# Kernel tuning notes

Hardware: AMD Instinct MI355X
Metric: run time of the kernel (lower is better)

The kernel has to match this reference:

```python
import jax, jax.numpy as jnp
import numpy as np

K = 3  # kernel size


def _qparams(t):
    # dynamic per-tensor affine quant params: scale=(max-min)/255, zero=-round(min/scale)
    mx = jnp.max(t)
    mn = jnp.min(t)
    s = (mx - mn) / 255.0
    z = -jnp.round(mn / s)
    return s, z


def _quant(t, s, z):
    return jnp.clip(jnp.round(t / s + z), 0.0, 255.0).astype(jnp.int32)


def setup_inputs() -> dict:
    key = jax.random.key(0)
    k1, k2, k3 = jax.random.split(key, 3)
    x = jax.random.normal(k1, (4, 32, 34, 34), dtype=jnp.float32)
    weight = jax.random.normal(k2, (64, 32, K, K), dtype=jnp.float32) * 0.1
    bias = jax.random.normal(k3, (64,), dtype=jnp.float32) * 0.1
    a = jnp.arange(256, dtype=jnp.float32)
    lut = a[:, None] * a[None, :]
    return {"x": x, "weight": weight, "lut": lut, "bias": bias}


def reference(x, weight, lut, bias):
    OC = weight.shape[0]
    # --- dynamic per-tensor quantization of activations and weights ---
    s_x, z_x = _qparams(x)
    s_w, z_w = _qparams(weight)
    qx = _quant(x, s_x, z_x)                       # [B, C, H, W] uint8 codes (int32)
    qw = _quant(weight, s_w, z_w).reshape(OC, -1)  # [OC, C*K*K]

    # --- im2col on the quantized activations (VALID, stride 1) ---
    patches = jax.lax.conv_general_dilated_patches(
        qx.astype(jnp.float32), (K, K), (1, 1), 'VALID')  # [B, C*K*K, OH, OW]
    B, CKK, OH, OW = patches.shape
    qxp = patches.astype(jnp.int32).transpose(0, 2, 3, 1).reshape(B, OH * OW, CKK)

    # --- LUT-based approximate multiply-accumulate ---
    # idx[b, p, oc, k] = qxp[b, p, k] * 256 + qw[oc, k]
    idx = qxp[:, :, None, :] * 256 + qw[None, None, :, :]          # [B, P, OC, CKK]
    acc = jnp.take(lut.reshape(-1), idx).sum(axis=-1)              # [B, P, OC]

    # --- affine dequantization of the integer accumulator ---
    sum_qw = qw.sum(axis=-1).astype(jnp.float32)                   # [OC]
    sum_qx = qxp.sum(axis=-1).astype(jnp.float32)                  # [B, P]
    out = s_x * s_w * (acc
                       - z_x * sum_qw[None, None, :]
                       - z_w * sum_qx[:, :, None]
                       + CKK * z_x * z_w)                          # [B, P, OC]
    out = out.reshape(B, OH, OW, OC).transpose(0, 3, 1, 2)         # [B, OC, OH, OW]
    return out + bias[None, :, None, None]
```

## Files before the change

kernel.cpp:

```cpp
#include <hip/hip_runtime.h>
#include <stdint.h>

#define B_    4
#define C_    32
#define HW_   34
#define OC_   64
#define CKK_  288

#define NX (B_*C_*HW_*HW_)
#define NW (OC_*C_*9)
#define NX4 (NX/4)
#define NW4 (NW/4)
#define NT4 (NX4+NW4)

__device__ __forceinline__ unsigned fmap(float f) {
  int i = __float_as_int(f);
  return (i < 0) ? ~(unsigned)i : ((unsigned)i | 0x80000000u);
}
__device__ __forceinline__ float funmap(unsigned u) {
  int i = (u & 0x80000000u) ? (int)(u ^ 0x80000000u) : ~(int)u;
  return __int_as_float(i);
}
__device__ __forceinline__ unsigned umax_(unsigned a, unsigned b){ return a>b?a:b; }
__device__ __forceinline__ unsigned umin_(unsigned a, unsigned b){ return a<b?a:b; }

__device__ __forceinline__ unsigned dot4(unsigned a, unsigned b, unsigned acc) {
#if __has_builtin(__builtin_amdgcn_udot4)
  return __builtin_amdgcn_udot4(a, b, acc, false);
#else
  acc += (a & 0xFFu) * (b & 0xFFu);
  acc += ((a >> 8) & 0xFFu) * ((b >> 8) & 0xFFu);
  acc += ((a >> 16) & 0xFFu) * ((b >> 16) & 0xFFu);
  acc += (a >> 24) * (b >> 24);
  return acc;
#endif
}

__global__ __launch_bounds__(256) void minmax_kernel(const float* __restrict__ x,
                                                     const float* __restrict__ w,
                                                     unsigned* __restrict__ ws) {
  unsigned xmax = 0, xnmin = 0, wmax = 0, wnmin = 0;
  int tid = blockIdx.x * 256 + threadIdx.x;
  int stride = gridDim.x * 256;
  for (int u = tid; u < NT4; u += stride) {
    bool isx = u < NX4;
    float4 v = isx ? ((const float4*)x)[u] : ((const float4*)w)[u - NX4];
    unsigned m0 = fmap(v.x), m1 = fmap(v.y), m2 = fmap(v.z), m3 = fmap(v.w);
    unsigned hi = umax_(umax_(m0, m1), umax_(m2, m3));
    unsigned lo = ~umin_(umin_(m0, m1), umin_(m2, m3));
    if (isx) { xmax = umax_(xmax, hi); xnmin = umax_(xnmin, lo); }
    else     { wmax = umax_(wmax, hi); wnmin = umax_(wnmin, lo); }
  }
  for (int m = 32; m; m >>= 1) {
    xmax  = umax_(xmax,  (unsigned)__shfl_xor((int)xmax,  m, 64));
    xnmin = umax_(xnmin, (unsigned)__shfl_xor((int)xnmin, m, 64));
    wmax  = umax_(wmax,  (unsigned)__shfl_xor((int)wmax,  m, 64));
    wnmin = umax_(wnmin, (unsigned)__shfl_xor((int)wnmin, m, 64));
  }
  __shared__ unsigned red[4][4];
  int wid = threadIdx.x >> 6, lane = threadIdx.x & 63;
  if (lane == 0) { red[wid][0] = xmax; red[wid][1] = xnmin; red[wid][2] = wmax; red[wid][3] = wnmin; }
  __syncthreads();
  if (threadIdx.x < 4) {
    unsigned v = umax_(umax_(red[0][threadIdx.x], red[1][threadIdx.x]),
                       umax_(red[2][threadIdx.x], red[3][threadIdx.x]));
    atomicMax(&ws[threadIdx.x], v);
  }
}

__global__ __launch_bounds__(256) void conv_kernel(const float* __restrict__ x,
                                                   const float* __restrict__ w,
                                                   const float* __restrict__ bias,
                                                   const unsigned* __restrict__ ws,
                                                   float* __restrict__ out) {
  const int och = blockIdx.x;
  const int oh  = blockIdx.y;
  const int b   = blockIdx.z;
  const int t   = threadIdx.x;

  const float mxx = funmap(ws[0]), mnx = funmap(~ws[1]);
  const float mxw = funmap(ws[2]), mnw = funmap(~ws[3]);
  const float s_x = (mxx - mnx) / 255.0f;
  const float z_x = -rintf(mnx / s_x);
  const float s_w = (mxw - mnw) / 255.0f;
  const float z_w = -rintf(mnw / s_w);

  __shared__ unsigned s_qw[32 * 32 * 4];
  __shared__ unsigned s_pt[32 * 32 * 4];
  __shared__ int s_sumqw[32];

  for (int i = t; i < 32 * 32 * 4; i += 256) { s_qw[i] = 0; s_pt[i] = 0; }
  __syncthreads();

  {
    const float* wsrc = w + och * (32 * CKK_);
    unsigned char* qb = (unsigned char*)s_qw;
    #pragma unroll
    for (int i = 0; i < 36; i++) {
      int idx = t + i * 256;
      float v = wsrc[idx] / s_w + z_w;
      int q = (int)rintf(v);
      q = min(max(q, 0), 255);
      int ocl = idx / CKK_;
      int k   = idx - ocl * CKK_;
      int c   = k / 9;
      int kr  = k - c * 9;
      int r   = kr / 3;
      int kw  = kr - r * 3;
      qb[(ocl * 32 + (c ^ ((ocl >> 1) & 7))) * 16 + r * 4 + kw] = (unsigned char)q;
    }
  }
  {
    const float* xsrc = x + (size_t)b * (C_ * HW_ * HW_);
    unsigned char* pb = (unsigned char*)s_pt;
    #pragma unroll
    for (int i = 0; i < 13; i++) {
      int idx = t + i * 256;
      if (idx < 32 * 3 * HW_) {
        int c   = idx / (3 * HW_);
        int rem = idx - c * (3 * HW_);
        int r   = rem / HW_;
        int wc  = rem - r * HW_;
        float v = xsrc[(c * HW_ + (oh + r)) * HW_ + wc] / s_x + z_x;
        int q = (int)rintf(v);
        q = min(max(q, 0), 255);
        #pragma unroll
        for (int kw = 0; kw < 3; kw++) {
          int ow = wc - kw;
          if (0 <= ow && ow < 32)
            pb[(ow * 32 + (c ^ ((ow >> 1) & 7))) * 16 + r * 4 + kw] = (unsigned char)q;
        }
      }
    }
  }
  __syncthreads();

  if (t < 32) {
    unsigned s = 0;
    const unsigned* row = s_qw + t * 128;
    for (int i = 0; i < 128; i++) s = dot4(row[i], 0x01010101u, s);
    s_sumqw[t] = (int)s;
  }

  const int owp = t & 15, ocp = t >> 4;
  const int ow0 = owp * 2, oc0 = ocp * 2;
  const unsigned psw = (unsigned)(owp & 7);
  const unsigned wsw = (unsigned)(ocp & 7);

  unsigned a00 = 0, a01 = 0, a10 = 0, a11 = 0, sx0 = 0, sx1 = 0;
  const uint4* qw4 = (const uint4*)s_qw;
  const uint4* pt4 = (const uint4*)s_pt;
  #pragma unroll 8
  for (int c = 0; c < 32; c++) {
    uint4 w0 = qw4[oc0 * 32 + (c ^ wsw)];
    uint4 w1 = qw4[(oc0 + 1) * 32 + (c ^ wsw)];
    uint4 p0 = pt4[ow0 * 32 + (c ^ psw)];
    uint4 p1 = pt4[(ow0 + 1) * 32 + (c ^ psw)];
    a00 = dot4(p0.x, w0.x, a00); a00 = dot4(p0.y, w0.y, a00); a00 = dot4(p0.z, w0.z, a00);
    a01 = dot4(p0.x, w1.x, a01); a01 = dot4(p0.y, w1.y, a01); a01 = dot4(p0.z, w1.z, a01);
    a10 = dot4(p1.x, w0.x, a10); a10 = dot4(p1.y, w0.y, a10); a10 = dot4(p1.z, w0.z, a10);
    a11 = dot4(p1.x, w1.x, a11); a11 = dot4(p1.y, w1.y, a11); a11 = dot4(p1.z, w1.z, a11);
    sx0 = dot4(p0.x, 0x01010101u, sx0); sx0 = dot4(p0.y, 0x01010101u, sx0); sx0 = dot4(p0.z, 0x01010101u, sx0);
    sx1 = dot4(p1.x, 0x01010101u, sx1); sx1 = dot4(p1.y, 0x01010101u, sx1); sx1 = dot4(p1.z, 0x01010101u, sx1);
  }
  __syncthreads();

  const float sxw = s_x * s_w;
  const float zz  = 288.0f * z_x * z_w;
  const int ocg0 = och * 32 + oc0;
  const float bz0 = bias[ocg0], bz1 = bias[ocg0 + 1];
  const float sqw0 = (float)s_sumqw[oc0], sqw1 = (float)s_sumqw[oc0 + 1];
  const float fs0 = (float)(int)sx0, fs1 = (float)(int)sx1;

  float2 r0, r1;
  r0.x = sxw * ((float)(int)a00 - z_x * sqw0 - z_w * fs0 + zz) + bz0;
  r0.y = sxw * ((float)(int)a10 - z_x * sqw0 - z_w * fs1 + zz) + bz0;
  r1.x = sxw * ((float)(int)a01 - z_x * sqw1 - z_w * fs0 + zz) + bz1;
  r1.y = sxw * ((float)(int)a11 - z_x * sqw1 - z_w * fs1 + zz) + bz1;

  float* obase = out + ((((size_t)b * OC_ + ocg0) * 32 + oh) * 32 + ow0);
  *(float2*)obase = r0;
  *(float2*)(obase + 32 * 32) = r1;
}

extern "C" void kernel_launch(void* const* d_in, const int* in_sizes, int n_in,
                              void* d_out, int out_size, void* d_ws, size_t ws_size,
                              hipStream_t stream) {
  const float* x    = (const float*)d_in[0];
  const float* w    = (const float*)d_in[1];
  const float* bias = (const float*)d_in[3];
  unsigned* ws = (unsigned*)d_ws;

  hipMemsetAsync(d_ws, 0, 16, stream);
  minmax_kernel<<<64, 256, 0, stream>>>(x, w, ws);
  dim3 grid(2, 32, 4);
  conv_kernel<<<grid, 256, 0, stream>>>(x, w, bias, ws, (float*)d_out);
}
```

Before: 78.40 us.

## Fuse min/max reduction into conv kernel with redundant per-block reduction

Drops the memset and the separate minmax kernel. Every conv block now redundantly reads all of x and w (~630KB) to compute the global quantization parameters in shared memory, then proceeds with the convolution. This removes two launches and the device-wide atomic handoff between them. In exchange, each of the 256 blocks repeats the full reduction, mostly served from L2.

```diff
diff --git a/kernel.cpp b/kernel.cpp
--- a/kernel.cpp
+++ b/kernel.cpp
@@ -36,13 +36,25 @@
 #endif
 }
 
-__global__ __launch_bounds__(256) void minmax_kernel(const float* __restrict__ x,
-                                                     const float* __restrict__ w,
-                                                     unsigned* __restrict__ ws) {
+__global__ __launch_bounds__(256) void fused_kernel(const float* __restrict__ x,
+                                                    const float* __restrict__ w,
+                                                    const float* __restrict__ bias,
+                                                    float* __restrict__ out) {
+  const int och = blockIdx.x;
+  const int oh  = blockIdx.y;
+  const int b   = blockIdx.z;
+  const int t   = threadIdx.x;
+
+  __shared__ unsigned s_qw[32 * 32 * 4];
+  __shared__ unsigned s_pt[32 * 32 * 4];
+  __shared__ int s_sumqw[32];
+  __shared__ unsigned red[4][4];
+  __shared__ float s_par[4];
+
+  for (int i = t; i < 32 * 32 * 4; i += 256) { s_qw[i] = 0; s_pt[i] = 0; }
+
   unsigned xmax = 0, xnmin = 0, wmax = 0, wnmin = 0;
-  int tid = blockIdx.x * 256 + threadIdx.x;
-  int stride = gridDim.x * 256;
-  for (int u = tid; u < NT4; u += stride) {
+  for (int u = t; u < NT4; u += 256) {
     bool isx = u < NX4;
     float4 v = isx ? ((const float4*)x)[u] : ((const float4*)w)[u - NX4];
     unsigned m0 = fmap(v.x), m1 = fmap(v.y), m2 = fmap(v.z), m3 = fmap(v.w);
@@ -57,40 +69,25 @@
     wmax  = umax_(wmax,  (unsigned)__shfl_xor((int)wmax,  m, 64));
     wnmin = umax_(wnmin, (unsigned)__shfl_xor((int)wnmin, m, 64));
   }
-  __shared__ unsigned red[4][4];
-  int wid = threadIdx.x >> 6, lane = threadIdx.x & 63;
+  const int wid = t >> 6, lane = t & 63;
   if (lane == 0) { red[wid][0] = xmax; red[wid][1] = xnmin; red[wid][2] = wmax; red[wid][3] = wnmin; }
   __syncthreads();
-  if (threadIdx.x < 4) {
-    unsigned v = umax_(umax_(red[0][threadIdx.x], red[1][threadIdx.x]),
-                       umax_(red[2][threadIdx.x], red[3][threadIdx.x]));
-    atomicMax(&ws[threadIdx.x], v);
+  if (t == 0) {
+    unsigned r0 = umax_(umax_(red[0][0], red[1][0]), umax_(red[2][0], red[3][0]));
+    unsigned r1 = umax_(umax_(red[0][1], red[1][1]), umax_(red[2][1], red[3][1]));
+    unsigned r2 = umax_(umax_(red[0][2], red[1][2]), umax_(red[2][2], red[3][2]));
+    unsigned r3 = umax_(umax_(red[0][3], red[1][3]), umax_(red[2][3], red[3][3]));
+    float mxx = funmap(r0), mnx = funmap(~r1);
+    float mxw = funmap(r2), mnw = funmap(~r3);
+    float sx = (mxx - mnx) / 255.0f;
+    float sw = (mxw - mnw) / 255.0f;
+    s_par[0] = sx;
+    s_par[1] = -rintf(mnx / sx);
+    s_par[2] = sw;
+    s_par[3] = -rintf(mnw / sw);
   }
-}
-
-__global__ __launch_bounds__(256) void conv_kernel(const float* __restrict__ x,
-                                                   const float* __restrict__ w,
-                                                   const float* __restrict__ bias,
-                                                   const unsigned* __restrict__ ws,
-                                                   float* __restrict__ out) {
-  const int och = blockIdx.x;
-  const int oh  = blockIdx.y;
-  const int b   = blockIdx.z;
-  const int t   = threadIdx.x;
-
-  const float mxx = funmap(ws[0]), mnx = funmap(~ws[1]);
-  const float mxw = funmap(ws[2]), mnw = funmap(~ws[3]);
-  const float s_x = (mxx - mnx) / 255.0f;
-  const float z_x = -rintf(mnx / s_x);
-  const float s_w = (mxw - mnw) / 255.0f;
-  const float z_w = -rintf(mnw / s_w);
-
-  __shared__ unsigned s_qw[32 * 32 * 4];
-  __shared__ unsigned s_pt[32 * 32 * 4];
-  __shared__ int s_sumqw[32];
-
-  for (int i = t; i < 32 * 32 * 4; i += 256) { s_qw[i] = 0; s_pt[i] = 0; }
   __syncthreads();
+  const float s_x = s_par[0], z_x = s_par[1], s_w = s_par[2], z_w = s_par[3];
 
   {
     const float* wsrc = w + och * (32 * CKK_);
@@ -189,10 +186,7 @@
   const float* x    = (const float*)d_in[0];
   const float* w    = (const float*)d_in[1];
   const float* bias = (const float*)d_in[3];
-  unsigned* ws = (unsigned*)d_ws;
 
-  hipMemsetAsync(d_ws, 0, 16, stream);
-  minmax_kernel<<<64, 256, 0, stream>>>(x, w, ws);
   dim3 grid(2, 32, 4);
-  conv_kernel<<<grid, 256, 0, stream>>>(x, w, bias, ws, (float*)d_out);
+  fused_kernel<<<grid, 256, 0, stream>>>(x, w, bias, (float*)d_out);
 }
```

New measurement: 104.0 us. 32.7% more time.
